# Kernel optimization log

Measured on AMD Instinct MI355X. Metric: run time of the kernel, lower is better.

## Reference

```python
import jax, jax.numpy as jnp
import numpy as np

N, D, E = 10000, 64, 32768   # nodes, padded degree, target edges
F, H, O = 64, 256, 1         # in_channels, hidden_channels, out_channels


def _linear_init(key, fin, fout):
    kw, kb = jax.random.split(key)
    s = 1.0 / np.sqrt(fin)
    w = jax.random.uniform(kw, (fin, fout), jnp.float32, -s, s)
    b = jax.random.uniform(kb, (fout,), jnp.float32, -s, s)
    return w, b


def setup_inputs() -> dict:
    key = jax.random.key(0)
    ks = jax.random.split(key, 12)
    x = jax.random.normal(ks[0], (N, F), jnp.float32)
    adj_nbr = jax.random.randint(ks[1], (N, D), 0, N)          # padded neighbor lists
    tar_ei = jax.random.randint(ks[2], (2, E), 0, N)           # target edges
    xcn_w1, xcn_b1 = _linear_init(ks[3], F, H)
    xcn_w2, xcn_b2 = _linear_init(ks[4], H, H)
    xcn_w3, xcn_b3 = _linear_init(ks[5], H, H)
    xij_w1, xij_b1 = _linear_init(ks[6], F, H)
    xij_w2, xij_b2 = _linear_init(ks[7], H, H)
    lin_w1, lin_b1 = _linear_init(ks[8], H, H)
    lin_w2, lin_b2 = _linear_init(ks[9], H, O)
    beta = jnp.ones((1,), jnp.float32)
    return dict(x=x, adj_nbr=adj_nbr, tar_ei=tar_ei, beta=beta,
                xcn_w1=xcn_w1, xcn_b1=xcn_b1, xcn_w2=xcn_w2, xcn_b2=xcn_b2,
                xcn_w3=xcn_w3, xcn_b3=xcn_b3,
                xij_w1=xij_w1, xij_b1=xij_b1, xij_w2=xij_w2, xij_b2=xij_b2,
                lin_w1=lin_w1, lin_b1=lin_b1, lin_w2=lin_w2, lin_b2=lin_b2)


def reference(x, adj_nbr, tar_ei, beta,
              xcn_w1, xcn_b1, xcn_w2, xcn_b2, xcn_w3, xcn_b3,
              xij_w1, xij_b1, xij_w2, xij_b2,
              lin_w1, lin_b1, lin_w2, lin_b2):
    relu = jax.nn.relu
    i, j = tar_ei[0], tar_ei[1]
    # adjoverlap: common-neighbor intersection of rows i and j of the adjacency
    ni = adj_nbr[i]                                   # [E, D] neighbors of i
    nj = adj_nbr[j]                                   # [E, D] neighbors of j
    cm = (ni[:, :, None] == nj[:, None, :]).any(-1)   # [E, D] ni[a] in N(j)?
    # spmm_add(cn, x): sum features of common neighbors per target edge
    xcn = jnp.einsum('ed,edf->ef', cm.astype(x.dtype), x[ni])  # [E, F]
    # xijlin(xi * xj): Linear -> ReLU -> Linear
    xij = x[i] * x[j]
    h_ij = relu(xij @ xij_w1 + xij_b1) @ xij_w2 + xij_b2
    # xcnlin(xcn): Linear -> ReLU -> Linear -> ReLU -> Linear
    h_cn = relu(xcn @ xcn_w1 + xcn_b1)
    h_cn = relu(h_cn @ xcn_w2 + xcn_b2)
    h_cn = h_cn @ xcn_w3 + xcn_b3
    # lin(xcnlin(xcn) * beta + xij): Linear -> ReLU -> Linear
    h = relu((h_cn * beta + h_ij) @ lin_w1 + lin_b1)
    return h @ lin_w2 + lin_b2                        # [E, O]
```

## Files before the change

kernel.cpp:

```cpp
#include <hip/hip_runtime.h>

#define NNODES 10000
#define DDEG   64
#define NEDGES 32768
#define FIN    64
#define HID    256

typedef __attribute__((ext_vector_type(8))) __bf16 bf16x8;
typedef __attribute__((ext_vector_type(4))) float  f32x4;

__device__ __forceinline__ unsigned short f2bf(float f) {
    unsigned x = __float_as_uint(f);
    return (unsigned short)((x + 0x7FFFu + ((x >> 16) & 1u)) >> 16);
}
__device__ __forceinline__ float b2f(unsigned short u) {
    return __uint_as_float(((unsigned)u) << 16);
}

#define OFF_XIJ1 0
#define OFF_XIJ2 16384
#define OFF_XCN1 81920
#define OFF_XCN2 98304
#define OFF_XCN3 163840
#define OFF_LIN1 229376
#define WT_TOTAL 294912
#define NTILES   36

__host__ __device__ constexpr int tile_off(int t) {
    return t < 2  ? OFF_XIJ1 + t * 8192
         : t < 10 ? OFF_XIJ2 + (t - 2) * 8192
         : t < 12 ? OFF_XCN1 + (t - 10) * 8192
         : t < 20 ? OFF_XCN2 + (t - 12) * 8192
         : t < 28 ? OFF_XCN3 + (t - 20) * 8192
         :          OFF_LIN1 + (t - 28) * 8192;
}

__device__ __forceinline__ void gll16(const unsigned short* g, unsigned short* l) {
    __builtin_amdgcn_global_load_lds(
        (const __attribute__((address_space(1))) unsigned int*)g,
        (__attribute__((address_space(3))) unsigned int*)l, 16, 0, 0);
}
__device__ __forceinline__ void stage_tile(const unsigned short* g, unsigned short* l,
                                           int tid, int wv) {
#pragma unroll
    for (int c = 0; c < 4; ++c)
        gll16(g + c * 2048 + tid * 8, l + c * 2048 + wv * 512);
}
__device__ __forceinline__ void stage_act(const unsigned short* g, unsigned short* l,
                                          int tid, int wv) {
#pragma unroll
    for (int c = 0; c < 2; ++c)
        gll16(g + c * 2048 + tid * 8, l + c * 2048 + wv * 512);
}

__global__ __launch_bounds__(256) void edge_prep_k(const float* __restrict__ x,
                                                   const int* __restrict__ adj,
                                                   const int* __restrict__ tar,
                                                   const float* __restrict__ xij_w1,
                                                   const float* __restrict__ xij_w2,
                                                   const float* __restrict__ xcn_w1,
                                                   const float* __restrict__ xcn_w2,
                                                   const float* __restrict__ xcn_w3,
                                                   const float* __restrict__ lin_w1,
                                                   unsigned short* __restrict__ WT,
                                                   unsigned short* __restrict__ xij_g,
                                                   unsigned short* __restrict__ xcn_g) {
    const int wv   = threadIdx.x >> 6;
    const int lane = threadIdx.x & 63;
    const int e    = blockIdx.x * 4 + wv;

    int i = tar[e];
    int j = tar[NEDGES + e];
    int ni = adj[i * DDEG + lane];
    int nj = adj[j * DDEG + lane];
    float xi = x[i * FIN + lane];
    float xj = x[j * FIN + lane];

    bool found = false;
#pragma unroll
    for (int b = 0; b < 64; ++b)
        found |= (ni == (int)__builtin_amdgcn_readlane(nj, b));
    unsigned long long m = __ballot(found);

    float acc = 0.f;
    while (m) {
        int a = __ffsll(m) - 1;
        m &= m - 1;
        int r = (int)__builtin_amdgcn_readlane(ni, a);
        acc += x[r * FIN + lane];
    }
    int sl = lane ^ ((e & 7) << 3);
    xij_g[(size_t)e * FIN + sl] = f2bf(xi * xj);
    xcn_g[(size_t)e * FIN + sl] = f2bf(acc);

    if (blockIdx.x < WT_TOTAL / 256) {
        int idx = blockIdx.x * 256 + threadIdx.x;
        const float* src;
        int r;
        if (idx < OFF_XIJ2)      { r = idx - OFF_XIJ1; src = xij_w1; }
        else if (idx < OFF_XCN1) { r = idx - OFF_XIJ2; src = xij_w2; }
        else if (idx < OFF_XCN2) { r = idx - OFF_XCN1; src = xcn_w1; }
        else if (idx < OFF_XCN3) { r = idx - OFF_XCN2; src = xcn_w2; }
        else if (idx < OFF_LIN1) { r = idx - OFF_XCN3; src = xcn_w3; }
        else                     { r = idx - OFF_LIN1; src = lin_w1; }
        int kb  = r >> 13;
        int n   = (r & 8191) >> 5;
        int klo = r & 31;
        WT[idx] = f2bf(src[(kb * 32 + klo) * HID + n]);
    }
}

template <int T0, int NT, int LDA>
__device__ __forceinline__ void run_phase(const unsigned short* As,
                                          unsigned short* ring,
                                          const unsigned short* __restrict__ WT,
                                          const unsigned short* __restrict__ restage_src,
                                          unsigned short* sX,
                                          int lr, int lg, int col0,
                                          int tid, int wv, f32x4 acc[4][4]) {
#pragma unroll
    for (int m = 0; m < 4; ++m)
#pragma unroll
        for (int n = 0; n < 4; ++n) acc[m][n] = (f32x4){0.f, 0.f, 0.f, 0.f};
    const int sw = (lr & 7) << 3;
#pragma unroll
    for (int s = 0; s < NT; ++s) {
        const int t = T0 + s;
        asm volatile("s_waitcnt vmcnt(0) lgkmcnt(0)" ::: "memory");
        __builtin_amdgcn_s_barrier();
        if (t + 1 < NTILES)
            stage_tile(WT + tile_off(t + 1), ring + ((t + 1) & 1) * 8192, tid, wv);
        if (restage_src && s == 0)
            stage_act(restage_src, sX, tid, wv);
        const unsigned short* cur = ring + (t & 1) * 8192;
        bf16x8 a[4], b[4];
#pragma unroll
        for (int n = 0; n < 4; ++n)
            b[n] = *reinterpret_cast<const bf16x8*>(&cur[(col0 + n * 16 + lr) * 32 + 8 * lg]);
#pragma unroll
        for (int m = 0; m < 4; ++m)
            a[m] = *reinterpret_cast<const bf16x8*>(
                &As[(m * 16 + lr) * LDA + ((s * 32 + 8 * lg) ^ sw)]);
        __builtin_amdgcn_s_setprio(1);
#pragma unroll
        for (int m = 0; m < 4; ++m)
#pragma unroll
            for (int n = 0; n < 4; ++n)
                acc[m][n] = __builtin_amdgcn_mfma_f32_16x16x32_bf16(a[m], b[n], acc[m][n], 0, 0, 0);
        __builtin_amdgcn_s_setprio(0);
    }
}

__global__ __launch_bounds__(256, 2) void mlp_k(const unsigned short* __restrict__ xij_g,
                                                const unsigned short* __restrict__ xcn_g,
                                                const unsigned short* __restrict__ WT,
                                                const float* __restrict__ xij_b1,
                                                const float* __restrict__ xij_b2,
                                                const float* __restrict__ xcn_b1,
                                                const float* __restrict__ xcn_b2,
                                                const float* __restrict__ xcn_b3,
                                                const float* __restrict__ lin_b1,
                                                const float* __restrict__ lin_w2,
                                                const float* __restrict__ lin_b2,
                                                const float* __restrict__ beta,
                                                float* __restrict__ out) {
    __shared__ unsigned short sX[64 * 64];
    __shared__ unsigned short sH[64 * 256];
    __shared__ unsigned short sB[2 * 8192];

    const int tid  = threadIdx.x;
    const int wv   = tid >> 6;
    const int lane = tid & 63;
    const int lr   = lane & 15;
    const int lg   = lane >> 4;
    const int col0 = wv * 64;
    const int row0 = blockIdx.x * 64;

    stage_act(xij_g + (size_t)row0 * FIN, sX, tid, wv);
    stage_tile(WT + tile_off(0), sB, tid, wv);
    const float betaf = beta[0];

    f32x4 acc[4][4];
    float bl[4];

    run_phase<0, 2, 64>(sX, sB, WT, nullptr, nullptr, lr, lg, col0, tid, wv, acc);
#pragma unroll
    for (int n = 0; n < 4; ++n) bl[n] = xij_b1[col0 + n * 16 + lr];
#pragma unroll
    for (int m = 0; m < 4; ++m)
#pragma unroll
        for (int n = 0; n < 4; ++n)
#pragma unroll
            for (int i = 0; i < 4; ++i) {
                int row = m * 16 + 4 * lg + i;
                int col = col0 + n * 16 + lr;
                sH[row * HID + (col ^ ((row & 7) << 3))] = f2bf(fmaxf(acc[m][n][i] + bl[n], 0.f));
            }

    run_phase<2, 8, 256>(sH, sB, WT, xcn_g + (size_t)row0 * FIN, sX, lr, lg, col0, tid, wv, acc);
#pragma unroll
    for (int n = 0; n < 4; ++n) bl[n] = xij_b2[col0 + n * 16 + lr];
    unsigned hij_lo[4][4], hij_hi[4][4];
#pragma unroll
    for (int m = 0; m < 4; ++m)
#pragma unroll
        for (int n = 0; n < 4; ++n) {
            hij_lo[m][n] = ((unsigned)f2bf(acc[m][n][1] + bl[n]) << 16) | f2bf(acc[m][n][0] + bl[n]);
            hij_hi[m][n] = ((unsigned)f2bf(acc[m][n][3] + bl[n]) << 16) | f2bf(acc[m][n][2] + bl[n]);
        }

    run_phase<10, 2, 64>(sX, sB, WT, nullptr, nullptr, lr, lg, col0, tid, wv, acc);
#pragma unroll
    for (int n = 0; n < 4; ++n) bl[n] = xcn_b1[col0 + n * 16 + lr];
#pragma unroll
    for (int m = 0; m < 4; ++m)
#pragma unroll
        for (int n = 0; n < 4; ++n)
#pragma unroll
            for (int i = 0; i < 4; ++i) {
                int row = m * 16 + 4 * lg + i;
                int col = col0 + n * 16 + lr;
                sH[row * HID + (col ^ ((row & 7) << 3))] = f2bf(fmaxf(acc[m][n][i] + bl[n], 0.f));
            }

    run_phase<12, 8, 256>(sH, sB, WT, nullptr, nullptr, lr, lg, col0, tid, wv, acc);
    asm volatile("s_waitcnt lgkmcnt(0)" ::: "memory");
    __builtin_amdgcn_s_barrier();
#pragma unroll
    for (int n = 0; n < 4; ++n) bl[n] = xcn_b2[col0 + n * 16 + lr];
#pragma unroll
    for (int m = 0; m < 4; ++m)
#pragma unroll
        for (int n = 0; n < 4; ++n)
#pragma unroll
            for (int i = 0; i < 4; ++i) {
                int row = m * 16 + 4 * lg + i;
                int col = col0 + n * 16 + lr;
                sH[row * HID + (col ^ ((row & 7) << 3))] = f2bf(fmaxf(acc[m][n][i] + bl[n], 0.f));
            }

    run_phase<20, 8, 256>(sH, sB, WT, nullptr, nullptr, lr, lg, col0, tid, wv, acc);
    asm volatile("s_waitcnt lgkmcnt(0)" ::: "memory");
    __builtin_amdgcn_s_barrier();
#pragma unroll
    for (int n = 0; n < 4; ++n) bl[n] = xcn_b3[col0 + n * 16 + lr];
#pragma unroll
    for (int m = 0; m < 4; ++m)
#pragma unroll
        for (int n = 0; n < 4; ++n) {
            float h0 = b2f((unsigned short)(hij_lo[m][n] & 0xFFFF));
            float h1 = b2f((unsigned short)(hij_lo[m][n] >> 16));
            float h2 = b2f((unsigned short)(hij_hi[m][n] & 0xFFFF));
            float h3 = b2f((unsigned short)(hij_hi[m][n] >> 16));
            float v0 = (acc[m][n][0] + bl[n]) * betaf + h0;
            float v1 = (acc[m][n][1] + bl[n]) * betaf + h1;
            float v2 = (acc[m][n][2] + bl[n]) * betaf + h2;
            float v3 = (acc[m][n][3] + bl[n]) * betaf + h3;
            int rb = m * 16 + 4 * lg;
            int col = col0 + n * 16 + lr;
            sH[(rb + 0) * HID + (col ^ (((rb + 0) & 7) << 3))] = f2bf(v0);
            sH[(rb + 1) * HID + (col ^ (((rb + 1) & 7) << 3))] = f2bf(v1);
            sH[(rb + 2) * HID + (col ^ (((rb + 2) & 7) << 3))] = f2bf(v2);
            sH[(rb + 3) * HID + (col ^ (((rb + 3) & 7) << 3))] = f2bf(v3);
        }

    run_phase<28, 8, 256>(sH, sB, WT, nullptr, nullptr, lr, lg, col0, tid, wv, acc);
#pragma unroll
    for (int n = 0; n < 4; ++n) bl[n] = lin_b1[col0 + n * 16 + lr];
    float w2l[4];
#pragma unroll
    for (int n = 0; n < 4; ++n) w2l[n] = lin_w2[col0 + n * 16 + lr];
    float* sRed = (float*)sX;
#pragma unroll
    for (int m = 0; m < 4; ++m) {
        float p[4] = {0.f, 0.f, 0.f, 0.f};
#pragma unroll
        for (int n = 0; n < 4; ++n)
#pragma unroll
            for (int i = 0; i < 4; ++i)
                p[i] += fmaxf(acc[m][n][i] + bl[n], 0.f) * w2l[n];
#pragma unroll
        for (int i = 0; i < 4; ++i) {
            float s = p[i];
            s += __shfl_xor(s, 1);
            s += __shfl_xor(s, 2);
            s += __shfl_xor(s, 4);
            s += __shfl_xor(s, 8);
            if (lr == 0) sRed[wv * 64 + m * 16 + 4 * lg + i] = s;
        }
    }
    __syncthreads();
    if (tid < 64)
        out[row0 + tid] = sRed[tid] + sRed[64 + tid] + sRed[128 + tid] + sRed[192 + tid] + lin_b2[0];
}

extern "C" void kernel_launch(void* const* d_in, const int* in_sizes, int n_in,
                              void* d_out, int out_size, void* d_ws, size_t ws_size,
                              hipStream_t stream) {
    const float* x      = (const float*)d_in[0];
    const int*   adj    = (const int*)d_in[1];
    const int*   tar    = (const int*)d_in[2];
    const float* beta   = (const float*)d_in[3];
    const float* xcn_w1 = (const float*)d_in[4];
    const float* xcn_b1 = (const float*)d_in[5];
    const float* xcn_w2 = (const float*)d_in[6];
    const float* xcn_b2 = (const float*)d_in[7];
    const float* xcn_w3 = (const float*)d_in[8];
    const float* xcn_b3 = (const float*)d_in[9];
    const float* xij_w1 = (const float*)d_in[10];
    const float* xij_b1 = (const float*)d_in[11];
    const float* xij_w2 = (const float*)d_in[12];
    const float* xij_b2 = (const float*)d_in[13];
    const float* lin_w1 = (const float*)d_in[14];
    const float* lin_b1 = (const float*)d_in[15];
    const float* lin_w2 = (const float*)d_in[16];
    const float* lin_b2 = (const float*)d_in[17];

    unsigned short* WT    = (unsigned short*)d_ws;
    unsigned short* xij_g = (unsigned short*)((char*)d_ws + 589824);
    unsigned short* xcn_g = (unsigned short*)((char*)d_ws + 4784128);

    edge_prep_k<<<NEDGES / 4, 256, 0, stream>>>(x, adj, tar,
                                                xij_w1, xij_w2, xcn_w1, xcn_w2, xcn_w3, lin_w1,
                                                WT, xij_g, xcn_g);
    mlp_k<<<NEDGES / 64, 256, 0, stream>>>(xij_g, xcn_g, WT,
                                           xij_b1, xij_b2, xcn_b1, xcn_b2, xcn_b3,
                                           lin_b1, lin_w2, lin_b2, beta, (float*)d_out);
}
```

Baseline: 65.45 us.

## Give each wave a private weight ring to drop per-tile block barriers

Each wave now stages only its own 64-column slice of every weight tile into a private double-buffered LDS ring. It waits on its own vmcnt instead of a block-wide barrier every k-step, so the per-tile s_barrier is removed. Block barriers now appear only at phase boundaries, where the activation buffers in sH/sX change hands. The launch bound drops the min-2-blocks hint, which may change register allocation and occupancy. The vmcnt(4) waits rely on exact in-order counting of the outstanding global_load_lds operations.

```diff
diff --git a/kernel.cpp b/kernel.cpp
--- a/kernel.cpp
+++ b/kernel.cpp
@@ -40,11 +40,11 @@
         (const __attribute__((address_space(1))) unsigned int*)g,
         (__attribute__((address_space(3))) unsigned int*)l, 16, 0, 0);
 }
-__device__ __forceinline__ void stage_tile(const unsigned short* g, unsigned short* l,
-                                           int tid, int wv) {
+__device__ __forceinline__ void stage_slice(const unsigned short* src, unsigned short* dst,
+                                            int lane) {
 #pragma unroll
     for (int c = 0; c < 4; ++c)
-        gll16(g + c * 2048 + tid * 8, l + c * 2048 + wv * 512);
+        gll16(src + c * 512 + lane * 8, dst + c * 512);
 }
 __device__ __forceinline__ void stage_act(const unsigned short* g, unsigned short* l,
                                           int tid, int wv) {
@@ -112,12 +112,10 @@
 
 template <int T0, int NT, int LDA>
 __device__ __forceinline__ void run_phase(const unsigned short* As,
-                                          unsigned short* ring,
+                                          unsigned short* myring,
                                           const unsigned short* __restrict__ WT,
-                                          const unsigned short* __restrict__ restage_src,
-                                          unsigned short* sX,
-                                          int lr, int lg, int col0,
-                                          int tid, int wv, f32x4 acc[4][4]) {
+                                          int myslice, int lr, int lg, int lane,
+                                          f32x4 acc[4][4]) {
 #pragma unroll
     for (int m = 0; m < 4; ++m)
 #pragma unroll
@@ -126,17 +124,17 @@
 #pragma unroll
     for (int s = 0; s < NT; ++s) {
         const int t = T0 + s;
-        asm volatile("s_waitcnt vmcnt(0) lgkmcnt(0)" ::: "memory");
-        __builtin_amdgcn_s_barrier();
         if (t + 1 < NTILES)
-            stage_tile(WT + tile_off(t + 1), ring + ((t + 1) & 1) * 8192, tid, wv);
-        if (restage_src && s == 0)
-            stage_act(restage_src, sX, tid, wv);
-        const unsigned short* cur = ring + (t & 1) * 8192;
+            stage_slice(WT + tile_off(t + 1) + myslice, myring + ((t + 1) & 1) * 2048, lane);
+        if (t + 1 < NTILES)
+            asm volatile("s_waitcnt vmcnt(4)" ::: "memory");
+        else
+            asm volatile("s_waitcnt vmcnt(0)" ::: "memory");
+        const unsigned short* cur = myring + (t & 1) * 2048;
         bf16x8 a[4], b[4];
 #pragma unroll
         for (int n = 0; n < 4; ++n)
-            b[n] = *reinterpret_cast<const bf16x8*>(&cur[(col0 + n * 16 + lr) * 32 + 8 * lg]);
+            b[n] = *reinterpret_cast<const bf16x8*>(&cur[(n * 16 + lr) * 32 + 8 * lg]);
 #pragma unroll
         for (int m = 0; m < 4; ++m)
             a[m] = *reinterpret_cast<const bf16x8*>(
@@ -151,22 +149,27 @@
     }
 }
 
-__global__ __launch_bounds__(256, 2) void mlp_k(const unsigned short* __restrict__ xij_g,
-                                                const unsigned short* __restrict__ xcn_g,
-                                                const unsigned short* __restrict__ WT,
-                                                const float* __restrict__ xij_b1,
-                                                const float* __restrict__ xij_b2,
-                                                const float* __restrict__ xcn_b1,
-                                                const float* __restrict__ xcn_b2,
-                                                const float* __restrict__ xcn_b3,
-                                                const float* __restrict__ lin_b1,
-                                                const float* __restrict__ lin_w2,
-                                                const float* __restrict__ lin_b2,
-                                                const float* __restrict__ beta,
-                                                float* __restrict__ out) {
+__device__ __forceinline__ void fence_barrier() {
+    asm volatile("s_waitcnt lgkmcnt(0)" ::: "memory");
+    __builtin_amdgcn_s_barrier();
+}
+
+__global__ __launch_bounds__(256) void mlp_k(const unsigned short* __restrict__ xij_g,
+                                             const unsigned short* __restrict__ xcn_g,
+                                             const unsigned short* __restrict__ WT,
+                                             const float* __restrict__ xij_b1,
+                                             const float* __restrict__ xij_b2,
+                                             const float* __restrict__ xcn_b1,
+                                             const float* __restrict__ xcn_b2,
+                                             const float* __restrict__ xcn_b3,
+                                             const float* __restrict__ lin_b1,
+                                             const float* __restrict__ lin_w2,
+                                             const float* __restrict__ lin_b2,
+                                             const float* __restrict__ beta,
+                                             float* __restrict__ out) {
     __shared__ unsigned short sX[64 * 64];
     __shared__ unsigned short sH[64 * 256];
-    __shared__ unsigned short sB[2 * 8192];
+    __shared__ unsigned short sBr[4 * 2 * 2048];
 
     const int tid  = threadIdx.x;
     const int wv   = tid >> 6;
@@ -175,15 +178,19 @@
     const int lg   = lane >> 4;
     const int col0 = wv * 64;
     const int row0 = blockIdx.x * 64;
+    const int myslice = wv * 2048;
+    unsigned short* myring = sBr + wv * 4096;
 
     stage_act(xij_g + (size_t)row0 * FIN, sX, tid, wv);
-    stage_tile(WT + tile_off(0), sB, tid, wv);
+    stage_slice(WT + tile_off(0) + myslice, myring, lane);
     const float betaf = beta[0];
+    asm volatile("s_waitcnt vmcnt(4)" ::: "memory");
+    __builtin_amdgcn_s_barrier();
 
     f32x4 acc[4][4];
     float bl[4];
 
-    run_phase<0, 2, 64>(sX, sB, WT, nullptr, nullptr, lr, lg, col0, tid, wv, acc);
+    run_phase<0, 2, 64>(sX, myring, WT, myslice, lr, lg, lane, acc);
 #pragma unroll
     for (int n = 0; n < 4; ++n) bl[n] = xij_b1[col0 + n * 16 + lr];
 #pragma unroll
@@ -196,8 +203,10 @@
                 int col = col0 + n * 16 + lr;
                 sH[row * HID + (col ^ ((row & 7) << 3))] = f2bf(fmaxf(acc[m][n][i] + bl[n], 0.f));
             }
-
-    run_phase<2, 8, 256>(sH, sB, WT, xcn_g + (size_t)row0 * FIN, sX, lr, lg, col0, tid, wv, acc);
+    fence_barrier();
+    stage_act(xcn_g + (size_t)row0 * FIN, sX, tid, wv);
+
+    run_phase<2, 8, 256>(sH, myring, WT, myslice, lr, lg, lane, acc);
 #pragma unroll
     for (int n = 0; n < 4; ++n) bl[n] = xij_b2[col0 + n * 16 + lr];
     unsigned hij_lo[4][4], hij_hi[4][4];
@@ -208,8 +217,9 @@
             hij_lo[m][n] = ((unsigned)f2bf(acc[m][n][1] + bl[n]) << 16) | f2bf(acc[m][n][0] + bl[n]);
             hij_hi[m][n] = ((unsigned)f2bf(acc[m][n][3] + bl[n]) << 16) | f2bf(acc[m][n][2] + bl[n]);
         }
-
-    run_phase<10, 2, 64>(sX, sB, WT, nullptr, nullptr, lr, lg, col0, tid, wv, acc);
+    fence_barrier();
+
+    run_phase<10, 2, 64>(sX, myring, WT, myslice, lr, lg, lane, acc);
 #pragma unroll
     for (int n = 0; n < 4; ++n) bl[n] = xcn_b1[col0 + n * 16 + lr];
 #pragma unroll
@@ -222,10 +232,10 @@
                 int col = col0 + n * 16 + lr;
                 sH[row * HID + (col ^ ((row & 7) << 3))] = f2bf(fmaxf(acc[m][n][i] + bl[n], 0.f));
             }
-
-    run_phase<12, 8, 256>(sH, sB, WT, nullptr, nullptr, lr, lg, col0, tid, wv, acc);
-    asm volatile("s_waitcnt lgkmcnt(0)" ::: "memory");
-    __builtin_amdgcn_s_barrier();
+    fence_barrier();
+
+    run_phase<12, 8, 256>(sH, myring, WT, myslice, lr, lg, lane, acc);
+    fence_barrier();
 #pragma unroll
     for (int n = 0; n < 4; ++n) bl[n] = xcn_b2[col0 + n * 16 + lr];
 #pragma unroll
@@ -238,10 +248,10 @@
                 int col = col0 + n * 16 + lr;
                 sH[row * HID + (col ^ ((row & 7) << 3))] = f2bf(fmaxf(acc[m][n][i] + bl[n], 0.f));
             }
-
-    run_phase<20, 8, 256>(sH, sB, WT, nullptr, nullptr, lr, lg, col0, tid, wv, acc);
-    asm volatile("s_waitcnt lgkmcnt(0)" ::: "memory");
-    __builtin_amdgcn_s_barrier();
+    fence_barrier();
+
+    run_phase<20, 8, 256>(sH, myring, WT, myslice, lr, lg, lane, acc);
+    fence_barrier();
 #pragma unroll
     for (int n = 0; n < 4; ++n) bl[n] = xcn_b3[col0 + n * 16 + lr];
 #pragma unroll
@@ -263,8 +273,9 @@
             sH[(rb + 2) * HID + (col ^ (((rb + 2) & 7) << 3))] = f2bf(v2);
             sH[(rb + 3) * HID + (col ^ (((rb + 3) & 7) << 3))] = f2bf(v3);
         }
-
-    run_phase<28, 8, 256>(sH, sB, WT, nullptr, nullptr, lr, lg, col0, tid, wv, acc);
+    fence_barrier();
+
+    run_phase<28, 8, 256>(sH, myring, WT, myslice, lr, lg, lane, acc);
 #pragma unroll
     for (int n = 0; n < 4; ++n) bl[n] = lin_b1[col0 + n * 16 + lr];
     float w2l[4];
```

Result: slower. 70.05 us (+7.0%).
